# Performance work log

Measured on AMD Instinct MI355X. Metric: run time of the kernel, lower is better.

## Reference

```python
import jax, jax.numpy as jnp
import numpy as np
import math

N_CELLS = 2048; HC_DIM = 11; HC_NODES = 2048
D = 1024; IN_DIM = 512; L = 2; H = 8; B = 2; HD = D // H
# XOR neighbor table: hypercube scatter-to-neighbor == gather-from-neighbor (involution)
NBR_WALK = jnp.asarray(np.arange(HC_NODES)[:, None] ^ (1 << np.arange(HC_DIM)))  # [Nn, hc_dim]
NB_INJ = min(HC_DIM, 6)
NB_FRUST = min(int(math.log2(N_CELLS)), 10)
FRUST_BITS = jnp.asarray(1 << np.arange(NB_FRUST))
N_MORPH = 48; N_FRUST_SAMPLES = min(N_CELLS, 128)


def _walk_step(amps, coin, x_mean):
    coined = jnp.einsum('ij,njd->nid', coin, amps)              # [Nn,2,D] complex
    new1 = coined[:, 1, :][NBR_WALK].sum(1) / HC_DIM            # XOR neighbor mix
    new = jnp.stack([coined[:, 0, :], new1], axis=1)
    new = new * jnp.exp(1j * (x_mean * 0.1))
    return new / (jnp.sqrt((jnp.abs(new) ** 2).sum()) + 1e-8)


def _inject(cells, amps):
    probs = (jnp.abs(amps) ** 2).sum((1, 2))
    probs = probs / (probs.sum() + 1e-8)
    ph = jnp.angle(amps.sum(1)).mean(-1)                        # [Nn]
    idx = jnp.arange(N_CELLS) % HC_NODES
    p = probs[idx]
    phc = ph[idx] * 0.3
    cells = cells * (0.8 + 0.4 * p)[:, None]
    c, s = jnp.cos(phc)[:, None], jnp.sin(phc)[:, None]
    h1, h2 = cells[:, :D // 2], cells[:, D // 2:]
    rot = jnp.concatenate([h1 * c - h2 * s, h1 * s + h2 * c], axis=1)
    cells = 0.5 * rot + 0.5 * cells
    nbr = idx[:, None] ^ (1 << jnp.arange(NB_INJ))              # [n_cells, 6]
    interf = ((p[:, None] - probs[nbr]) * 0.03).sum(1)
    return cells + interf[:, None]


def _frustration(cells, fsigns):
    # sequential in torch (cells[j] may already be updated for j<i) -> fori_loop
    def body(i, cells):
        j = i ^ FRUST_BITS
        valid = (j < N_CELLS).astype(cells.dtype)
        sign = fsigns[i] * fsigns[j] * valid
        infl = (sign[:, None] * cells[j]).sum(0)
        cnt = valid.sum()
        return cells.at[i].set(0.85 * cells[i] + 0.15 * infl / jnp.maximum(cnt, 1.0))
    return jax.lax.fori_loop(0, N_FRUST_SAMPLES, body, cells)


def _standing_wave(cells, step):
    i = jnp.arange(N_CELLS, dtype=cells.dtype)
    fwd = (step * 0.15) % N_CELLS
    bwd = (N_CELLS - step * 0.15) % N_CELLS
    amp = 1.0 / jnp.cosh((i - fwd) / 2) ** 2 + 1.0 / jnp.cosh((i - bwd) / 2) ** 2
    return cells * (1.0 + 0.03 * amp)[:, None]


def _morphism(cells):
    # torch hs[j] are views, so updates are visible sequentially -> fori_loop
    def body(i, cells):
        ms = jnp.tanh(cells[:N_MORPH] - cells[i]).sum(0) / (N_MORPH - 1)  # tanh(0)=0 handles j==i
        return cells.at[i].set(0.9 * cells[i] + 0.1 * ms)
    return jax.lax.fori_loop(0, N_MORPH, body, cells)


def _faction(cells, step, sync=0.15, debate=0.15, n_f=8):
    fsz = N_CELLS // n_f
    h = cells.reshape(n_f, fsz, D)
    h = (1 - sync) * h + sync * h.mean(1, keepdims=True)
    if step > 5:
        g = h.mean(1).mean(0)
        dc = max(1, fsz // 4)
        h = h.at[:, :dc].set((1 - debate) * h[:, :dc] + debate * g)
    return h.reshape(N_CELLS, D)


def _ln(x, g, b, eps=1e-5):
    mu = x.mean(-1, keepdims=True)
    v = ((x - mu) ** 2).mean(-1, keepdims=True)
    return (x - mu) / jnp.sqrt(v + eps) * g + b


def _update_cells(cells, amp_real, amp_imag, coin_real, coin_imag, fsigns, x, step):
    amps = amp_real + 1j * amp_imag
    coin = coin_real + 1j * coin_imag
    x_mean = x.mean()
    for _ in range(2):  # process() runs walk+inject twice
        amps = _walk_step(amps, coin, x_mean)
        cells = _inject(cells, amps)
    cells = _frustration(cells, fsigns)
    cells = _standing_wave(cells, step)
    if step % 3 == 0:
        cells = _morphism(cells)
    return _faction(cells, step)


def _forward(x, amp_real, amp_imag, coin_real, coin_imag, cell_embeddings, frustration_signs,
             w_in, b_in, attn_in_w, attn_in_b, attn_out_w, attn_out_b, ln_g, ln_b, w_out, b_out, step):
    upd = jax.lax.stop_gradient(_update_cells(
        cell_embeddings, amp_real, amp_imag, coin_real, coin_imag, frustration_signs, x, step))
    # straight-through: torch mutates .data in place, Parameter grad flows through updated values
    cells0 = cell_embeddings + jax.lax.stop_gradient(upd - cell_embeddings)
    x_proj = x @ w_in.T + b_in                                   # [B, D]
    cells = cells0[None] + x_proj[:, None] * 0.1                 # [B, S, D]
    tension = jnp.float32(0.0)
    for l in range(L):
        qkv = cells @ attn_in_w[l].T + attn_in_b[l]
        q, k, v = jnp.split(qkv, 3, axis=-1)
        q = q.reshape(B, N_CELLS, H, HD).transpose(0, 2, 1, 3)
        k = k.reshape(B, N_CELLS, H, HD).transpose(0, 2, 1, 3)
        v = v.reshape(B, N_CELLS, H, HD).transpose(0, 2, 1, 3)
        attn = jax.nn.softmax(jnp.einsum('bhqd,bhkd->bhqk', q, k) / math.sqrt(HD), axis=-1)
        out = jnp.einsum('bhqk,bhkd->bhqd', attn, v).transpose(0, 2, 1, 3).reshape(B, N_CELLS, D)
        out = out @ attn_out_w[l].T + attn_out_b[l]
        cells = _ln(cells + out, ln_g[l], ln_b[l])
        tension = tension + jnp.std(attn.mean(1), ddof=1)        # torch MHA averages heads; std unbiased
    tension = tension / L
    output = cells @ w_out.T + b_out                             # [B, S, IN_DIM]
    return output, tension


def setup_inputs():
    key = jax.random.key(0)
    ks = jax.random.split(key, 12)
    x = jax.random.normal(ks[0], (B, IN_DIM), jnp.float32)
    ar = jax.random.normal(ks[1], (HC_NODES, 2, D), jnp.float32) * 0.1
    ai = jax.random.normal(ks[2], (HC_NODES, 2, D), jnp.float32) * 0.1
    nrm = jnp.sqrt((ar ** 2 + ai ** 2).sum()) + 1e-8
    cells = jax.random.normal(ks[3], (N_CELLS, D), jnp.float32) * 0.1
    perm = jax.random.permutation(ks[4], N_CELLS)
    fsigns = jnp.ones(N_CELLS, jnp.float32).at[perm[:N_CELLS // 2]].set(-1.0)
    s = 1.0 / math.sqrt(D)
    return dict(
        x=x, amp_real=ar / nrm, amp_imag=ai / nrm,
        coin_real=jnp.array([[1.0, 1.0], [1.0, -1.0]], jnp.float32) / math.sqrt(2),
        coin_imag=jnp.zeros((2, 2), jnp.float32),
        cell_embeddings=cells, frustration_signs=fsigns,
        w_in=jax.random.normal(ks[5], (D, IN_DIM), jnp.float32) / math.sqrt(IN_DIM),
        b_in=jnp.zeros(D, jnp.float32),
        attn_in_w=jax.random.normal(ks[6], (L, 3 * D, D), jnp.float32) * s,
        attn_in_b=jnp.zeros((L, 3 * D), jnp.float32),
        attn_out_w=jax.random.normal(ks[7], (L, D, D), jnp.float32) * s,
        attn_out_b=jnp.zeros((L, D), jnp.float32),
        ln_g=jnp.ones((L, D), jnp.float32), ln_b=jnp.zeros((L, D), jnp.float32),
        w_out=jax.random.normal(ks[8], (IN_DIM, D), jnp.float32) * s,
        b_out=jnp.zeros(IN_DIM, jnp.float32),
        step=6)


def reference(x, amp_real, amp_imag, coin_real, coin_imag, cell_embeddings, frustration_signs,
              w_in, b_in, attn_in_w, attn_in_b, attn_out_w, attn_out_b, ln_g, ln_b, w_out, b_out, step):
    return _forward(x, amp_real, amp_imag, coin_real, coin_imag, cell_embeddings, frustration_signs,
                    w_in, b_in, attn_in_w, attn_in_b, attn_out_w, attn_out_b, ln_g, ln_b, w_out, b_out, step)
```

## Files before the change

### kernel.cpp

```cpp
#include <hip/hip_runtime.h>

#define U16 unsigned short

typedef short bf16x8 __attribute__((ext_vector_type(8)));
typedef float f32x4 __attribute__((ext_vector_type(4)));

__device__ __forceinline__ float bfp(const U16* p) { return __uint_as_float(((unsigned)(*p)) << 16); }
__device__ __forceinline__ U16 f2bf(float f) {
  unsigned u = __float_as_uint(f);
  u += 0x7FFFu + ((u >> 16) & 1u);
  return (U16)(u >> 16);
}
__device__ __forceinline__ float ldv(const void* p, long i, bool bf) {
  return bf ? bfp((const U16*)p + i) : ((const float*)p)[i];
}
__device__ __forceinline__ void gload_lds16(const U16* g, U16* l) {
  __builtin_amdgcn_global_load_lds((const __attribute__((address_space(1))) void*)g,
                                   (__attribute__((address_space(3))) void*)l, 16, 0, 0);
}


__global__ __launch_bounds__(256) void init_kernel(const void* __restrict__ x, const U16* __restrict__ lng,
                                                   float* __restrict__ scal) {
  __shared__ float red[256];
  __shared__ int fl;
  int t = threadIdx.x;
  if (t == 0) fl = (lng[0] != 0) ? 1 : 0;
  __syncthreads();
  bool bf = fl != 0;
  float s = 0.f;
  for (int i = t; i < 1024; i += 256) s += ldv(x, i, bf);
  red[t] = s; __syncthreads();
  for (int o = 128; o; o >>= 1) { if (t < o) red[t] += red[t + o]; __syncthreads(); }
  if (t == 0) { scal[0] = red[0] * (1.f / 1024.f); scal[16] = bf ? 1.f : 0.f; }
  else if (t < 64 && t != 16) scal[t] = 0.f;
}

__global__ __launch_bounds__(256) void walk_coined_kernel(const void* __restrict__ arv, const void* __restrict__ aiv,
                                                          float* __restrict__ cr, float* __restrict__ ci,
                                                          const void* __restrict__ coinR, const void* __restrict__ coinI,
                                                          const float* __restrict__ scal, int iter) {
  bool bf = scal[16] != 0.f;
  int id = blockIdx.x * 256 + threadIdx.x;
  int n = id >> 10, d = id & 1023;
  size_t b0 = (size_t)n * 2048 + d;
  float pre = 1.f;
  float a0r, a0i, a1r, a1i;
  if (iter == 0) {
    a0r = ldv(arv, b0, bf); a1r = ldv(arv, b0 + 1024, bf);
    a0i = ldv(aiv, b0, bf); a1i = ldv(aiv, b0 + 1024, bf);
  } else {
    pre = 1.f / (sqrtf(scal[iter]) + 1e-8f);
    const float* ar = (const float*)arv;
    const float* ai = (const float*)aiv;
    a0r = ar[b0]; a1r = ar[b0 + 1024]; a0i = ai[b0]; a1i = ai[b0 + 1024];
  }
  a0r *= pre; a0i *= pre; a1r *= pre; a1i *= pre;
  float c00r = ldv(coinR, 0, bf), c01r = ldv(coinR, 1, bf), c10r = ldv(coinR, 2, bf), c11r = ldv(coinR, 3, bf);
  float c00i = ldv(coinI, 0, bf), c01i = ldv(coinI, 1, bf), c10i = ldv(coinI, 2, bf), c11i = ldv(coinI, 3, bf);
  cr[b0]        = c00r * a0r - c00i * a0i + c01r * a1r - c01i * a1i;
  ci[b0]        = c00r * a0i + c00i * a0r + c01r * a1i + c01i * a1r;
  cr[b0 + 1024] = c10r * a0r - c10i * a0i + c11r * a1r - c11i * a1i;
  ci[b0 + 1024] = c10r * a0i + c10i * a0r + c11r * a1i + c11i * a1r;
}

__global__ __launch_bounds__(256) void walk_new_stats_kernel(const float* __restrict__ cr, const float* __restrict__ ci,
                                                             float* __restrict__ ar, float* __restrict__ ai,
                                                             const float* __restrict__ scal, float* __restrict__ scalw,
                                                             int slot, float* __restrict__ probs, float* __restrict__ ph) {
  __shared__ float r1[256], r2[256];
  int n = blockIdx.x, t = threadIdx.x;
  float th = scal[0] * 0.1f;
  float sn, cs; sincosf(th, &sn, &cs);
  float pacc = 0.f, phacc = 0.f;
  #pragma unroll
  for (int it = 0; it < 4; ++it) {
    int d = t + it * 256;
    size_t b0 = (size_t)n * 2048 + d;
    float n0r = cr[b0], n0i = ci[b0];
    float s1r = 0.f, s1i = 0.f;
    #pragma unroll
    for (int k = 0; k < 11; ++k) {
      size_t j = (size_t)(n ^ (1 << k)) * 2048 + 1024 + d;
      s1r += cr[j]; s1i += ci[j];
    }
    s1r *= (1.f / 11.f); s1i *= (1.f / 11.f);
    float o0r = n0r * cs - n0i * sn, o0i = n0r * sn + n0i * cs;
    float o1r = s1r * cs - s1i * sn, o1i = s1r * sn + s1i * cs;
    ar[b0] = o0r; ai[b0] = o0i; ar[b0 + 1024] = o1r; ai[b0 + 1024] = o1i;
    pacc += o0r * o0r + o0i * o0i + o1r * o1r + o1i * o1i;
    phacc += atan2f(o0i + o1i, o0r + o1r);
  }
  r1[t] = pacc; r2[t] = phacc; __syncthreads();
  for (int o = 128; o; o >>= 1) { if (t < o) { r1[t] += r1[t + o]; r2[t] += r2[t + o]; } __syncthreads(); }
  if (t == 0) { probs[n] = r1[0]; ph[n] = r2[0] * (1.f / 1024.f); atomicAdd(&scalw[slot], r1[0]); }
}

__global__ __launch_bounds__(256) void inject_cells_kernel(const void* __restrict__ cellsIn, float* __restrict__ cells,
                                                           const float* __restrict__ probs,
                                                           const float* __restrict__ ph, const float* __restrict__ scal,
                                                           int wslot, int useRaw) {
  bool bf = scal[16] != 0.f;
  int id = blockIdx.x * 256 + threadIdx.x;
  int c = id >> 9, d = id & 511;
  float invn = 1.f / (sqrtf(scal[wslot]) + 1e-8f);
  float inv2 = invn * invn;
  float denom = 1.f / (scal[wslot] * inv2 + 1e-8f);
  float psc = inv2 * denom;
  float p = probs[c] * psc;
  float interf = 0.f;
  #pragma unroll
  for (int j = 0; j < 6; ++j) interf += (p - probs[c ^ (1 << j)] * psc);
  interf *= 0.03f;
  float scale = 0.8f + 0.4f * p;
  float phc = ph[c] * 0.3f;
  float sn, cs; sincosf(phc, &sn, &cs);
  size_t base = (size_t)c * 1024 + d;
  float h1, h2;
  if (useRaw) { h1 = ldv(cellsIn, base, bf) * scale; h2 = ldv(cellsIn, base + 512, bf) * scale; }
  else        { h1 = cells[base] * scale;            h2 = cells[base + 512] * scale; }
  float r1 = h1 * cs - h2 * sn, r2 = h1 * sn + h2 * cs;
  cells[base]       = 0.5f * (r1 + h1) + interf;
  cells[base + 512] = 0.5f * (r2 + h2) + interf;
}

__global__ __launch_bounds__(64) void frustration_kernel(float* __restrict__ cells, const void* __restrict__ fs,
                                                         const float* __restrict__ scal) {
  bool bf = scal[16] != 0.f;
  int d = blockIdx.x;
  int l = threadIdx.x;
  float s0 = ldv(fs, l, bf);
  float s1 = ldv(fs, l + 64, bf);
  float w0 = s0 * cells[(size_t)l * 1024 + d];
  float w1 = s1 * cells[(size_t)(l + 64) * 1024 + d];
  float stat0 = 0.f, stat1 = 0.f;
  #pragma unroll
  for (int b = 7; b < 10; ++b) {
    int j0 = l ^ (1 << b);
    int j1 = (l + 64) ^ (1 << b);
    stat0 += ldv(fs, j0, bf) * cells[(size_t)j0 * 1024 + d];
    stat1 += ldv(fs, j1, bf) * cells[(size_t)j1 * 1024 + d];
  }
  #pragma unroll
  for (int i = 0; i < 128; ++i) {
    const int hi = i >> 6;
    const int li = i & 63;
    float vsrc = (hi == 0) ? w0 : w1;
    float voth = (hi == 0) ? w1 : w0;
    float acc = __shfl(vsrc, li ^ 1) + __shfl(vsrc, li ^ 2) + __shfl(vsrc, li ^ 4)
              + __shfl(vsrc, li ^ 8) + __shfl(vsrc, li ^ 16) + __shfl(vsrc, li ^ 32)
              + __shfl(voth, li);
    if (l == li) {
      if (hi == 0) w0 = 0.85f * w0 + 0.015f * (acc + stat0);
      else         w1 = 0.85f * w1 + 0.015f * (acc + stat1);
    }
  }
  cells[(size_t)l * 1024 + d]        = s0 * w0;
  cells[(size_t)(l + 64) * 1024 + d] = s1 * w1;
}

__global__ __launch_bounds__(256) void standing_kernel(float* __restrict__ cells, const int* __restrict__ stepp) {
  int id = blockIdx.x * 256 + threadIdx.x;
  int c = id >> 10;
  float st = (float)stepp[0] * 0.15f;
  float fwd = fmodf(st, 2048.f);
  float bwd = fmodf(2048.f - st, 2048.f);
  float fi = (float)c;
  float r1 = 1.f / coshf((fi - fwd) * 0.5f);
  float r2 = 1.f / coshf((fi - bwd) * 0.5f);
  cells[id] *= (1.f + 0.03f * (r1 * r1 + r2 * r2));
}

__global__ __launch_bounds__(64) void morphism_kernel(float* __restrict__ cells, const int* __restrict__ stepp) {
  if (stepp[0] % 3 != 0) return;
  int d = blockIdx.x;
  int l = threadIdx.x;
  float v = 0.f;
  if (l < 48) v = cells[(size_t)l * 1024 + d];
  for (int i = 0; i < 48; ++i) {
    float vi = __shfl(v, i);
    float x = v - vi;
    float e2 = __expf(2.f * x);
    float th = (l < 48) ? (1.f - 2.f / (e2 + 1.f)) : 0.f;
    th += __shfl_xor(th, 1);
    th += __shfl_xor(th, 2);
    th += __shfl_xor(th, 4);
    th += __shfl_xor(th, 8);
    th += __shfl_xor(th, 16);
    th += __shfl_xor(th, 32);
    if (l == i) v = 0.9f * v + (0.1f / 47.f) * th;
  }
  if (l < 48) cells[(size_t)l * 1024 + d] = v;
}

__global__ __launch_bounds__(256) void faction_mean_kernel(const float* __restrict__ cells, float* __restrict__ fmean) {
  int id = blockIdx.x * 256 + threadIdx.x;
  int f = id >> 10, d = id & 1023;
  float s = 0.f;
  for (int r = 0; r < 256; ++r) s += cells[(size_t)((f << 8) + r) * 1024 + d];
  fmean[id] = s * (1.f / 256.f);
}
__global__ __launch_bounds__(256) void faction_apply_kernel(float* __restrict__ cells, const float* __restrict__ fmean,
                                                            const int* __restrict__ stepp) {
  int id = blockIdx.x * 256 + threadIdx.x;
  int c = id >> 10, d = id & 1023;
  int f = c >> 8, r = c & 255;
  float v = 0.85f * cells[id] + 0.15f * fmean[f * 1024 + d];
  if (stepp[0] > 5 && r < 64) {
    float g = 0.f;
    #pragma unroll
    for (int ff = 0; ff < 8; ++ff) g += fmean[ff * 1024 + d];
    v = 0.85f * v + 0.15f * g * 0.125f;
  }
  cells[id] = v;
}

__global__ __launch_bounds__(256) void xproj_kernel(const void* __restrict__ x, const void* __restrict__ w_in,
                                                    const void* __restrict__ b_in, float* __restrict__ xp,
                                                    const float* __restrict__ scal) {
  bool bf = scal[16] != 0.f;
  int id = blockIdx.x * 256 + threadIdx.x;
  int b = id >> 10, o = id & 1023;
  float acc = ldv(b_in, o, bf);
  if (bf) {
    const U16* xr = (const U16*)x + b * 512;
    const U16* wr = (const U16*)w_in + (long)o * 512;
    for (int k = 0; k < 512; ++k) acc += bfp(xr + k) * bfp(wr + k);
  } else {
    const float* xr = (const float*)x + b * 512;
    const float* wr = (const float*)w_in + (long)o * 512;
    for (int k = 0; k < 512; ++k) acc += xr[k] * wr[k];
  }
  xp[id] = acc;
}

__global__ __launch_bounds__(256) void cellsB_kernel(const float* __restrict__ cells, const float* __restrict__ xp,
                                                     float* __restrict__ cellsB, U16* __restrict__ cellsB16) {
  int id = blockIdx.x * 256 + threadIdx.x;
  int b = id >> 21;
  int cd = id & ((1 << 21) - 1);
  int d = id & 1023;
  float v = cells[cd] + 0.1f * xp[(b << 10) + d];
  cellsB[id] = v;
  cellsB16[id] = f2bf(v);
}

__global__ __launch_bounds__(256) void wcvt_kernel(const void* __restrict__ W, long off,
                                                   U16* __restrict__ dst, int n4,
                                                   const float* __restrict__ scal) {
  if (scal[16] != 0.f) return;
  int id = blockIdx.x * 256 + threadIdx.x;
  if (id < n4) {
    const float* src = (const float*)W + off;
    float4 v = *(const float4*)&src[(size_t)id * 4];
    ushort4 o;
    o.x = f2bf(v.x); o.y = f2bf(v.y); o.z = f2bf(v.z); o.w = f2bf(v.w);
    *(ushort4*)&dst[(size_t)id * 4] = o;
  }
}

__global__ __launch_bounds__(256) void mfma_gemm_kernel(const U16* __restrict__ A16,
                                                        const void* __restrict__ Wv, long Woff,
                                                        const U16* __restrict__ W16s,
                                                        const void* __restrict__ biasv, long Boff,
                                                        void* __restrict__ Cout, int N, int mode,
                                                        const float* __restrict__ scal) {
  __shared__ U16 Al[4096];
  __shared__ U16 Wl[4096];
  bool bf = scal[16] != 0.f;
  const int K = 1024;
  int t = threadIdx.x;
  int wv = t >> 6, l = t & 63;
  int n0 = blockIdx.x * 128, m0 = blockIdx.y * 128;
  int wmt = (wv & 1) * 4;
  int wnt = (wv >> 1) * 4;
  const U16* Wb = bf ? (const U16*)Wv + Woff : W16s;

  int fr0 = wv * 2, fr1 = fr0 + 1;
  const U16* asrc0 = A16 + (size_t)(m0 + fr0 * 16 + (l & 15)) * K + (l >> 4) * 8;
  const U16* asrc1 = A16 + (size_t)(m0 + fr1 * 16 + (l & 15)) * K + (l >> 4) * 8;
  const U16* wsrc0 = Wb  + (size_t)(n0 + fr0 * 16 + (l & 15)) * K + (l >> 4) * 8;
  const U16* wsrc1 = Wb  + (size_t)(n0 + fr1 * 16 + (l & 15)) * K + (l >> 4) * 8;
  U16* adst0 = &Al[fr0 * 512];
  U16* adst1 = &Al[fr1 * 512];
  U16* wdst0 = &Wl[fr0 * 512];
  U16* wdst1 = &Wl[fr1 * 512];

  f32x4 acc[4][4];
  #pragma unroll
  for (int i = 0; i < 4; ++i)
    #pragma unroll
    for (int j = 0; j < 4; ++j) acc[i][j] = (f32x4){0.f, 0.f, 0.f, 0.f};

  for (int k0 = 0; k0 < K; k0 += 32) {
    __syncthreads();
    gload_lds16(asrc0 + k0, adst0);
    gload_lds16(asrc1 + k0, adst1);
    gload_lds16(wsrc0 + k0, wdst0);
    gload_lds16(wsrc1 + k0, wdst1);
    __syncthreads();
    bf16x8 afr[4], bfr[4];
    #pragma unroll
    for (int i = 0; i < 4; ++i) afr[i] = *(const bf16x8*)&Al[((wmt + i) * 64 + l) * 8];
    #pragma unroll
    for (int j = 0; j < 4; ++j) bfr[j] = *(const bf16x8*)&Wl[((wnt + j) * 64 + l) * 8];
    #pragma unroll
    for (int i = 0; i < 4; ++i)
      #pragma unroll
      for (int j = 0; j < 4; ++j)
        acc[i][j] = __builtin_amdgcn_mfma_f32_16x16x32_bf16(afr[i], bfr[j], acc[i][j], 0, 0, 0);
  }
  bool outBf = (mode == 1) || (mode == 2 && bf);
  int cl = l & 15, rq = l >> 4;
  #pragma unroll
  for (int j = 0; j < 4; ++j) {
    int n = n0 + (wnt + j) * 16 + cl;
    float bv = ldv(biasv, Boff + n, bf);
    #pragma unroll
    for (int i = 0; i < 4; ++i) {
      int mrow = m0 + (wmt + i) * 16 + rq * 4;
      #pragma unroll
      for (int r = 0; r < 4; ++r) {
        float v = acc[i][j][r] + bv;
        if (outBf) ((U16*)Cout)[(size_t)(mrow + r) * N + n] = f2bf(v);
        else       ((float*)Cout)[(size_t)(mrow + r) * N + n] = v;
      }
    }
  }
}

__global__ __launch_bounds__(256) void pack_kv_kernel(const U16* __restrict__ qkv,
                                                      U16* __restrict__ Kp, U16* __restrict__ Vp) {
  __shared__ U16 tile[64][132];
  int t = threadIdx.x;
  int kc = blockIdx.x, bh = blockIdx.y;
  int b = bh >> 3, h = bh & 7;
  size_t dstB = ((size_t)bh * 32 + kc) * 8192;
  if (blockIdx.z == 0) {
    int w = t >> 6, l = t & 63;
    int l16 = l & 15, quad = l >> 4;
    #pragma unroll
    for (int fi = 0; fi < 4; ++fi) {
      int f = w * 4 + fi;
      int nt = f >> 2, kf = f & 3;
      const U16* src = qkv + ((size_t)(b * 2048 + kc * 64 + nt * 16 + l16)) * 3072 + 1024 + h * 128 + kf * 32 + quad * 8;
      *(uint4*)(Kp + dstB + (size_t)f * 512 + l * 8) = *(const uint4*)src;
    }
  } else {
    int r = t >> 2, c0 = (t & 3) * 32;
    const U16* src = qkv + ((size_t)(b * 2048 + kc * 64 + r)) * 3072 + 2048 + h * 128 + c0;
    #pragma unroll
    for (int q = 0; q < 8; ++q)
      *(ushort4*)&tile[r][c0 + q * 4] = *(const ushort4*)(src + q * 4);
    __syncthreads();
    #pragma unroll
    for (int i = 0; i < 4; ++i) {
      int p = t + 256 * i;
      int g = p >> 6, l = p & 63;
      int l16 = l & 15, quad = l >> 4;
      int nt = g >> 1, kf = g & 1;
      U16 vals[8];
      #pragma unroll
      for (int j = 0; j < 8; ++j) vals[j] = tile[kf * 32 + quad * 8 + j][nt * 16 + l16];
      *(uint4*)(Vp + dstB + (size_t)g * 512 + l * 8) = *(const uint4*)vals;
    }
  }
}

__global__ __launch_bounds__(256) void zero_zg_kernel(float* __restrict__ zg) {
  int id = blockIdx.x * 256 + threadIdx.x;
  if (id < 294912) zg[id] = 0.f;
}

#define EHST 1040
#define EBST (8 * EHST)
__global__ __launch_bounds__(1024, 4) void attn_mfma_kernel(U16* __restrict__ qkv,
                                                            const U16* __restrict__ Kp, const U16* __restrict__ Vp,
                                                            float* __restrict__ O32a,
                                                            float* __restrict__ zg) {
  __shared__ U16 ebuf[2 * EBST];
  int t = threadIdx.x;
  int w16 = t >> 6;
  int h = w16 & 7;
  int l = t & 63;
  int l16 = l & 15, quad = l >> 4;
  int idx = blockIdx.x;
  int khalf = idx & 1;
  int b = (idx >> 1) & 1;
  int q0 = (idx >> 2) * 32;
  size_t rowB = (size_t)b * 2048;
  const float sc = 0.08838834764831845f;
  const int c0 = khalf * 32, cend = c0 + 32;

  if (w16 < 8) {
    const U16* KpB = Kp + (size_t)(b * 8 + h) * 262144;
    bf16x8 afr[2][4];
    #pragma unroll
    for (int s = 0; s < 2; ++s) {
      const U16* Qb = qkv + (rowB + q0 + s * 16 + l16) * 3072 + h * 128 + quad * 8;
      #pragma unroll
      for (int kf = 0; kf < 4; ++kf) afr[s][kf] = *(const bf16x8*)(Qb + kf * 32);
    }
    f32x4 gacc[2];
    gacc[0] = (f32x4){0.f, 0.f, 0.f, 0.f};
    gacc[1] = (f32x4){0.f, 0.f, 0.f, 0.f};
    float zacc[2][4] = {{0.f, 0.f, 0.f, 0.f}, {0.f, 0.f, 0.f, 0.f}};
    bf16x8 bK[2][4];

    auto kload = [&](int c) {
      int kc64 = c >> 1, nh = (c & 1) * 2;
      #pragma unroll
      for (int i = 0; i < 2; ++i)
        #pragma unroll
        for (int kf = 0; kf < 4; ++kf)
          bK[i][kf] = *(const bf16x8*)(KpB + (size_t)kc64 * 8192 + (size_t)((nh + i) * 4 + kf) * 512 + l * 8);
    };
    auto produce = [&](int c) {
      f32x4 sacc[2][2];
      #pragma unroll
      for (int s = 0; s < 2; ++s)
        #pragma unroll
        for (int i = 0; i < 2; ++i) {
          sacc[s][i] = (f32x4){0.f, 0.f, 0.f, 0.f};
          #pragma unroll
          for (int kf = 0; kf < 4; ++kf)
            sacc[s][i] = __builtin_amdgcn_mfma_f32_16x16x32_bf16(afr[s][kf], bK[i][kf], sacc[s][i], 0, 0, 0);
        }
      U16* eb = &ebuf[(c & 1) * EBST + h * EHST];
      #pragma unroll
      for (int s = 0; s < 2; ++s) {
        #pragma unroll
        for (int i = 0; i < 2; ++i) {
          int kq = i * 2 + (l16 >> 3);
          int j = l16 & 7;
          #pragma unroll
          for (int r = 0; r < 4; ++r) {
            float e = __expf(fminf(sacc[s][i][r] * sc, 30.f));
            zacc[s][r] += e;
            eb[s * 512 + kq * 128 + (quad * 4 + r) * 8 + j] = f2bf(e);
          }
        }
      }
    };

    kload(c0);
    produce(c0);
    if (c0 + 1 < cend) kload(c0 + 1);

    for (int c = c0; c < cend; ++c) {
      __syncthreads();
      if (c + 1 < cend) {
        produce(c + 1);
        if (c + 2 < cend) kload(c + 2);
      }
      const U16* gb = &ebuf[(c & 1) * EBST];
      #pragma unroll
      for (int s = 0; s < 2; ++s) {
        bf16x8 gfr = *(const bf16x8*)(gb + (size_t)(l & 7) * EHST + s * 512
                                      + (quad * 16 + h * 2 + ((l >> 3) & 1)) * 8);
        gacc[s] = __builtin_amdgcn_mfma_f32_16x16x32_bf16(gfr, gfr, gacc[s], 0, 0, 0);
      }
    }
    #pragma unroll
    for (int s = 0; s < 2; ++s)
      #pragma unroll
      for (int r = 0; r < 4; ++r) {
        float z = zacc[s][r];
        z += __shfl_xor(z, 1); z += __shfl_xor(z, 2);
        z += __shfl_xor(z, 4); z += __shfl_xor(z, 8);
        zacc[s][r] = z;
      }
    if (l16 == 0) {
      #pragma unroll
      for (int s = 0; s < 2; ++s)
        #pragma unroll
        for (int r = 0; r < 4; ++r) {
          size_t m = rowB + q0 + s * 16 + quad * 4 + r;
          atomicAdd(&zg[m * 8 + h], zacc[s][r]);
        }
    }
    {
      int h2 = l16 & 7, b2 = l16 >> 3;
      int a = quad >> 1;
      if (a == b2) {
        float* G = zg + 32768;
        #pragma unroll
        for (int s = 0; s < 2; ++s) {
          size_t m = rowB + q0 + s * 16 + h * 2 + a;
          #pragma unroll
          for (int r = 0; r < 4; ++r) {
            int h1 = (quad * 4 + r) & 7;
            atomicAdd(&G[m * 64 + h1 * 8 + h2], gacc[s][r]);
          }
        }
      }
    }
  } else {
    const U16* VpB = Vp + (size_t)(b * 8 + h) * 262144;
    f32x4 oacc[2][8];
    #pragma unroll
    for (int s = 0; s < 2; ++s)
      #pragma unroll
      for (int i = 0; i < 8; ++i) oacc[s][i] = (f32x4){0.f, 0.f, 0.f, 0.f};
    bf16x8 bV[8];

    auto vload = [&](int c) {
      int kc64 = c >> 1, vk = c & 1;
      #pragma unroll
      for (int nt = 0; nt < 8; ++nt)
        bV[nt] = *(const bf16x8*)(VpB + (size_t)kc64 * 8192 + (size_t)(nt * 2 + vk) * 512 + l * 8);
    };

    vload(c0);
    for (int c = c0; c < cend; ++c) {
      __syncthreads();
      const U16* eb = &ebuf[(c & 1) * EBST + h * EHST];
      #pragma unroll
      for (int s = 0; s < 2; ++s) {
        bf16x8 pfr = *(const bf16x8*)&eb[s * 512 + l * 8];
        #pragma unroll
        for (int nt = 0; nt < 8; ++nt)
          oacc[s][nt] = __builtin_amdgcn_mfma_f32_16x16x32_bf16(pfr, bV[nt], oacc[s][nt], 0, 0, 0);
      }
      if (c + 1 < cend) vload(c + 1);
    }
    #pragma unroll
    for (int s = 0; s < 2; ++s)
      #pragma unroll
      for (int r = 0; r < 4; ++r) {
        size_t m = rowB + q0 + s * 16 + quad * 4 + r;
        float* orow;
        if (khalf == 0) orow = O32a + m * 1024 + h * 128 + l16;
        else            orow = (float*)(qkv + m * 3072 + 1024) + h * 128 + l16;
        #pragma unroll
        for (int nt = 0; nt < 8; ++nt) orow[nt * 16] = oacc[s][nt][r];
      }
  }
}

__global__ __launch_bounds__(256) void attn_norm_kernel(const float* __restrict__ O32a, const U16* __restrict__ qkv,
                                                        const float* __restrict__ zg, U16* __restrict__ O16) {
  int id = blockIdx.x * 256 + threadIdx.x;
  int base = id * 4;
  int m = base >> 10, d = base & 1023;
  const float* ob = (const float*)(qkv + (size_t)m * 3072 + 1024);
  float4 a = *(const float4*)&O32a[base];
  float4 bv = *(const float4*)&ob[d];
  float inv = 1.f / zg[m * 8 + (d >> 7)];
  ushort4 o;
  o.x = f2bf((a.x + bv.x) * inv);
  o.y = f2bf((a.y + bv.y) * inv);
  o.z = f2bf((a.z + bv.z) * inv);
  o.w = f2bf((a.w + bv.w) * inv);
  *(ushort4*)&O16[base] = o;
}

__global__ __launch_bounds__(256) void gram_fin_kernel(const float* __restrict__ zg, float* __restrict__ scal, int slot) {
  __shared__ float red[256];
  int t = threadIdx.x;
  const float* G = zg + 32768;
  float s = 0.f;
  for (int i = blockIdx.x * 256 * 16 + t; i < (blockIdx.x + 1) * 256 * 16; i += 256) {
    int m = i >> 6, h1 = (i >> 3) & 7, h2 = i & 7;
    s += G[i] / (zg[m * 8 + h1] * zg[m * 8 + h2]);
  }
  red[t] = s; __syncthreads();
  for (int o = 128; o; o >>= 1) { if (t < o) red[t] += red[t + o]; __syncthreads(); }
  if (t == 0) atomicAdd(&scal[slot], red[0] * (1.f / 64.f) - (blockIdx.x == 0 ? 2.0f : 0.0f));
}

__global__ __launch_bounds__(256) void ln_kernel(float* __restrict__ cellsB, U16* __restrict__ cellsB16,
                                                 const float* __restrict__ proj,
                                                 const void* __restrict__ gv, const void* __restrict__ bv, long off,
                                                 const float* __restrict__ scal) {
  __shared__ float red[256];
  bool bf = scal[16] != 0.f;
  int row = blockIdx.x, t = threadIdx.x;
  size_t base = (size_t)row * 1024;
  int d = 4 * t;
  float4 cv = *(const float4*)&cellsB[base + d];
  float4 pv = *(const float4*)&proj[base + d];
  float v0 = cv.x + pv.x, v1 = cv.y + pv.y, v2 = cv.z + pv.z, v3 = cv.w + pv.w;
  red[t] = v0 + v1 + v2 + v3; __syncthreads();
  for (int o = 128; o; o >>= 1) { if (t < o) red[t] += red[t + o]; __syncthreads(); }
  float mu = red[0] * (1.f / 1024.f);
  __syncthreads();
  float d0 = v0 - mu, d1 = v1 - mu, d2 = v2 - mu, d3 = v3 - mu;
  red[t] = d0 * d0 + d1 * d1 + d2 * d2 + d3 * d3; __syncthreads();
  for (int o = 128; o; o >>= 1) { if (t < o) red[t] += red[t + o]; __syncthreads(); }
  float rstd = rsqrtf(red[0] * (1.f / 1024.f) + 1e-5f);
  float4 out;
  out.x = d0 * rstd * ldv(gv, off + d, bf)     + ldv(bv, off + d, bf);
  out.y = d1 * rstd * ldv(gv, off + d + 1, bf) + ldv(bv, off + d + 1, bf);
  out.z = d2 * rstd * ldv(gv, off + d + 2, bf) + ldv(bv, off + d + 2, bf);
  out.w = d3 * rstd * ldv(gv, off + d + 3, bf) + ldv(bv, off + d + 3, bf);
  *(float4*)&cellsB[base + d] = out;
  ushort4 ob;
  ob.x = f2bf(out.x); ob.y = f2bf(out.y); ob.z = f2bf(out.z); ob.w = f2bf(out.w);
  *(ushort4*)&cellsB16[base + d] = ob;
}

__global__ void tension_kernel(const float* __restrict__ scal, void* __restrict__ out) {
  bool bf = scal[16] != 0.f;
  float cnt = 8388608.f;
  float ten = 0.f;
  for (int l = 0; l < 2; ++l) {
    float v = scal[8 + l] / (cnt - 1.f);
    ten += sqrtf(fmaxf(v, 0.f));
  }
  ten *= 0.5f;
  if (bf) ((U16*)out)[2097152] = f2bf(ten);
  else    ((float*)out)[2097152] = ten;
}

extern "C" void kernel_launch(void* const* d_in, const int* in_sizes, int n_in,
                              void* d_out, int out_size, void* d_ws, size_t ws_size,
                              hipStream_t stream) {
  const void* X    = d_in[0];
  const void* AR   = d_in[1];
  const void* AI   = d_in[2];
  const void* CRc  = d_in[3];
  const void* CIc  = d_in[4];
  const void* CE   = d_in[5];
  const void* FS   = d_in[6];
  const void* WIN  = d_in[7];
  const void* BIN  = d_in[8];
  const void* AIW  = d_in[9];
  const void* AIB  = d_in[10];
  const void* AOW  = d_in[11];
  const void* AOB  = d_in[12];
  const void* LNG  = d_in[13];
  const void* LNB  = d_in[14];
  const void* WOUT = d_in[15];
  const void* BOUT = d_in[16];
  const int* STEP  = (const int*)d_in[17];

  float* ws = (float*)d_ws;
  float* scal  = ws;
  float* probs = ws + 64;
  float* ph    = ws + 64 + 2048;
  float* fmean = ws + 64 + 4096;
  float* xp    = ws + 64 + 12288;
  float* cells = ws + 16384;
  float* CB    = ws + 16384 + 2097152;
  float* ar = CB;
  float* ai = CB + 4194304;
  float* cr = CB + 8388608;
  float* ci = CB + 12582912;
  float* cellsB   = CB;
  U16*   qkv16    = (U16*)(CB + 4194304);
  float* proj     = CB + 4194304;
  float* O32a     = CB + 10485760;
  U16*   cellsB16 = (U16*)(CB + 12582912);
  U16*   Kp       = (U16*)(CB + 14680064);
  U16*   Vp       = (U16*)cells;
  U16*   O16      = Kp;
  float* zg       = (float*)d_out;
  U16*   Wd16     = (U16*)d_out;
  U16*   WOUT16   = (U16*)proj;

  init_kernel<<<1, 256, 0, stream>>>(X, (const U16*)LNG, scal);

  for (int w = 0; w < 2; ++w) {
    if (w == 0) walk_coined_kernel<<<8192, 256, 0, stream>>>(AR, AI, cr, ci, CRc, CIc, scal, 0);
    else        walk_coined_kernel<<<8192, 256, 0, stream>>>(ar, ai, cr, ci, CRc, CIc, scal, 1);
    walk_new_stats_kernel<<<2048, 256, 0, stream>>>(cr, ci, ar, ai, scal, scal, 1 + w, probs, ph);
    inject_cells_kernel<<<4096, 256, 0, stream>>>(w == 0 ? CE : (const void*)cells, cells,
                                                  probs, ph, scal, 1 + w, w == 0 ? 1 : 0);
  }
  frustration_kernel<<<1024, 64, 0, stream>>>(cells, FS, scal);
  standing_kernel<<<8192, 256, 0, stream>>>(cells, STEP);
  morphism_kernel<<<1024, 64, 0, stream>>>(cells, STEP);
  faction_mean_kernel<<<32, 256, 0, stream>>>(cells, fmean);
  faction_apply_kernel<<<8192, 256, 0, stream>>>(cells, fmean, STEP);

  xproj_kernel<<<8, 256, 0, stream>>>(X, WIN, BIN, xp, scal);
  cellsB_kernel<<<16384, 256, 0, stream>>>(cells, xp, cellsB, cellsB16);

  for (int l = 0; l < 2; ++l) {
    wcvt_kernel<<<3072, 256, 0, stream>>>(AIW, (long)l * 3072 * 1024, Wd16, 786432, scal);
    mfma_gemm_kernel<<<dim3(24, 32), 256, 0, stream>>>(cellsB16, AIW, (long)l * 3072 * 1024, Wd16,
                                                       AIB, (long)l * 3072, qkv16, 3072, 1, scal);
    pack_kv_kernel<<<dim3(32, 16, 2), 256, 0, stream>>>(qkv16, Kp, Vp);
    zero_zg_kernel<<<1152, 256, 0, stream>>>(zg);
    attn_mfma_kernel<<<256, 1024, 0, stream>>>(qkv16, Kp, Vp, O32a, zg);
    attn_norm_kernel<<<4096, 256, 0, stream>>>(O32a, qkv16, zg, O16);
    gram_fin_kernel<<<64, 256, 0, stream>>>(zg, scal, 8 + l);
    wcvt_kernel<<<1024, 256, 0, stream>>>(AOW, (long)l * 1024 * 1024, Wd16, 262144, scal);
    mfma_gemm_kernel<<<dim3(8, 32), 256, 0, stream>>>(O16, AOW, (long)l * 1024 * 1024, Wd16,
                                                      AOB, (long)l * 1024, proj, 1024, 0, scal);
    ln_kernel<<<4096, 256, 0, stream>>>(cellsB, cellsB16, proj, LNG, LNB, (long)l * 1024, scal);
  }
  wcvt_kernel<<<512, 256, 0, stream>>>(WOUT, 0, WOUT16, 131072, scal);
  mfma_gemm_kernel<<<dim3(4, 32), 256, 0, stream>>>(cellsB16, WOUT, 0, WOUT16,
                                                    BOUT, 0, d_out, 512, 2, scal);
  tension_kernel<<<1, 1, 0, stream>>>(scal, d_out);
}
```

Measured before the change: 766.3 us.

## Triple-buffer LDS tiles in MFMA GEMM to overlap global loads with compute

Replaces the single-buffered LDS staging in the bf16 MFMA GEMM with a three-stage ring that prefetches two K-steps ahead. Explicit vmcnt waits and raw barriers replace the two __syncthreads per iteration, so the direct-to-LDS loads can overlap the MFMA work. It triples LDS use per block (48 KB), which can lower occupancy. It also depends on hand-counted vmcnt values matching the outstanding loads.

```diff
diff --git a/kernel.cpp b/kernel.cpp
--- a/kernel.cpp
+++ b/kernel.cpp
@@ -265,10 +265,11 @@
                                                         const void* __restrict__ biasv, long Boff,
                                                         void* __restrict__ Cout, int N, int mode,
                                                         const float* __restrict__ scal) {
-  __shared__ U16 Al[4096];
-  __shared__ U16 Wl[4096];
+  __shared__ U16 Al[3][4096];
+  __shared__ U16 Wl[3][4096];
   bool bf = scal[16] != 0.f;
   const int K = 1024;
+  const int NSTEP = 32;
   int t = threadIdx.x;
   int wv = t >> 6, l = t & 63;
   int n0 = blockIdx.x * 128, m0 = blockIdx.y * 128;
@@ -281,10 +282,13 @@
   const U16* asrc1 = A16 + (size_t)(m0 + fr1 * 16 + (l & 15)) * K + (l >> 4) * 8;
   const U16* wsrc0 = Wb  + (size_t)(n0 + fr0 * 16 + (l & 15)) * K + (l >> 4) * 8;
   const U16* wsrc1 = Wb  + (size_t)(n0 + fr1 * 16 + (l & 15)) * K + (l >> 4) * 8;
-  U16* adst0 = &Al[fr0 * 512];
-  U16* adst1 = &Al[fr1 * 512];
-  U16* wdst0 = &Wl[fr0 * 512];
-  U16* wdst1 = &Wl[fr1 * 512];
+
+  auto stage = [&](int buf, int k0) {
+    gload_lds16(asrc0 + k0, &Al[buf][fr0 * 512]);
+    gload_lds16(asrc1 + k0, &Al[buf][fr1 * 512]);
+    gload_lds16(wsrc0 + k0, &Wl[buf][fr0 * 512]);
+    gload_lds16(wsrc1 + k0, &Wl[buf][fr1 * 512]);
+  };
 
   f32x4 acc[4][4];
   #pragma unroll
@@ -292,24 +296,35 @@
     #pragma unroll
     for (int j = 0; j < 4; ++j) acc[i][j] = (f32x4){0.f, 0.f, 0.f, 0.f};
 
-  for (int k0 = 0; k0 < K; k0 += 32) {
-    __syncthreads();
-    gload_lds16(asrc0 + k0, adst0);
-    gload_lds16(asrc1 + k0, adst1);
-    gload_lds16(wsrc0 + k0, wdst0);
-    gload_lds16(wsrc1 + k0, wdst1);
-    __syncthreads();
+  stage(0, 0);
+  stage(1, 32);
+
+  for (int s = 0; s < NSTEP; ++s) {
+    if (s + 2 < NSTEP) {
+      stage((s + 2) % 3, (s + 2) * 32);
+      asm volatile("s_waitcnt vmcnt(8)" ::: "memory");
+    } else if (s + 1 < NSTEP) {
+      asm volatile("s_waitcnt vmcnt(4)" ::: "memory");
+    } else {
+      asm volatile("s_waitcnt vmcnt(0)" ::: "memory");
+    }
+    __builtin_amdgcn_s_barrier();
+    asm volatile("" ::: "memory");
+    int cb = s % 3;
     bf16x8 afr[4], bfr[4];
     #pragma unroll
-    for (int i = 0; i < 4; ++i) afr[i] = *(const bf16x8*)&Al[((wmt + i) * 64 + l) * 8];
-    #pragma unroll
-    for (int j = 0; j < 4; ++j) bfr[j] = *(const bf16x8*)&Wl[((wnt + j) * 64 + l) * 8];
+    for (int i = 0; i < 4; ++i) afr[i] = *(const bf16x8*)&Al[cb][((wmt + i) * 64 + l) * 8];
+    #pragma unroll
+    for (int j = 0; j < 4; ++j) bfr[j] = *(const bf16x8*)&Wl[cb][((wnt + j) * 64 + l) * 8];
     #pragma unroll
     for (int i = 0; i < 4; ++i)
       #pragma unroll
       for (int j = 0; j < 4; ++j)
         acc[i][j] = __builtin_amdgcn_mfma_f32_16x16x32_bf16(afr[i], bfr[j], acc[i][j], 0, 0, 0);
-  }
+    __builtin_amdgcn_s_barrier();
+    asm volatile("" ::: "memory");
+  }
+
   bool outBf = (mode == 1) || (mode == 2 && bf);
   int cl = l & 15, rq = l >> 4;
   #pragma unroll
```

Result: slower. 781.7 us, median of 2 (+2.0%).
